# Kernel optimization log

Measured on AMD Instinct MI355X. Metric: run time of the kernel, lower is better.

The kernel has to match this reference:

```python
import jax, jax.numpy as jnp
import numpy as np

D_CONV = 4
DT_RANK = 64
D_STATE = 16

def silu(v):
    return v * jax.nn.sigmoid(v)

def setup_inputs() -> dict:
    key = jax.random.key(0)
    ks = jax.random.split(key, 10)
    B, L, d_model, d_inner = 2, 2048, 1024, 2048
    def nrm(k, shape, scale):
        return jax.random.normal(k, shape, dtype=jnp.float32) * scale
    A = jnp.tile(jnp.arange(1, D_STATE + 1, dtype=jnp.float32), (d_inner, 1))
    return {
        'x': nrm(ks[0], (B, L, d_model), 1.0),
        'W_in': nrm(ks[1], (d_model, 2 * d_inner), d_model ** -0.5),
        'conv_w': nrm(ks[2], (d_inner, D_CONV), D_CONV ** -0.5),
        'conv_b': nrm(ks[3], (d_inner,), 0.02),
        'W_x': nrm(ks[4], (d_inner, DT_RANK + 2 * D_STATE), d_inner ** -0.5),
        'W_dt': nrm(ks[5], (DT_RANK, d_inner), DT_RANK ** -0.5),
        'b_dt': nrm(ks[6], (d_inner,), 0.02),
        'A_log': jnp.log(A),
        'D': jnp.ones((d_inner,), dtype=jnp.float32),
        'W_out': nrm(ks[7], (d_inner, d_model), d_inner ** -0.5),
    }

def reference(x, W_in, conv_w, conv_b, W_x, W_dt, b_dt, A_log, D, W_out):
    B, L, _ = x.shape
    d_inner = W_dt.shape[1]
    # input projection and gate split
    xz = x @ W_in                                   # [B, L, 2*d_inner]
    xb, z = jnp.split(xz, 2, axis=-1)
    # causal depthwise conv1d (pad left d_conv-1, then first L outputs)
    xp = jnp.pad(xb, ((0, 0), (D_CONV - 1, 0), (0, 0)))
    xc = sum(xp[:, k:k + L, :] * conv_w[:, k] for k in range(D_CONV)) + conv_b
    xb = silu(xc)                                   # [B, L, d_inner]
    # data-dependent SSM parameters
    x_dbl = xb @ W_x                                # [B, L, dt_rank + 2*d_state]
    dt_low, Bm, Cm = jnp.split(x_dbl, [DT_RANK, DT_RANK + D_STATE], axis=-1)
    dt = jax.nn.softplus(dt_low @ W_dt + b_dt)      # [B, L, d_inner]
    A = -jnp.exp(A_log)                             # [d_inner, d_state]

    def step(h, inp):
        dt_t, B_t, C_t, x_t = inp                   # [B,d_inner],[B,n],[B,n],[B,d_inner]
        dA = jnp.exp(A * dt_t[..., None])           # [B, d_inner, d_state]
        h = h * dA + (x_t * dt_t)[..., None] * B_t[:, None, :]
        y = jnp.einsum('bdn,bn->bd', h, C_t)
        return h, y

    xs = (dt.swapaxes(0, 1), Bm.swapaxes(0, 1), Cm.swapaxes(0, 1), xb.swapaxes(0, 1))
    h0 = jnp.zeros((B, d_inner, D_STATE), dtype=x.dtype)
    _, ys = jax.lax.scan(step, h0, xs)              # ys: [L, B, d_inner]
    y = ys.swapaxes(0, 1) + xb * D
    out = y * silu(z)
    return out @ W_out
```

## Files before the change

kernel.cpp:

```cpp
#include <hip/hip_runtime.h>
#include <hip/hip_bf16.h>


#define BATCH   2
#define SEQLEN  2048
#define DMODEL  1024
#define DINNER  2048
#define DCONV   4
#define DTRANK  64
#define DSTATE  16
#define BL      (BATCH * SEQLEN)
#define NXZ     (2 * DINNER)
#define XDBL_N  (DTRANK + 2 * DSTATE)
#define LCH     32
#define NCHUNK  (SEQLEN / LCH)
#define KSPLIT  8
#define KC      (DINNER / KSPLIT)
#define KS_OUT  4
#define KCO     (DINNER / KS_OUT)
#define KS_XD   8
#define KCX     (DINNER / KS_XD)
#define XDP     128

typedef __bf16 bf16x8 __attribute__((ext_vector_type(8)));
typedef __bf16 bf16x4 __attribute__((ext_vector_type(4)));
typedef float  floatx4 __attribute__((ext_vector_type(4)));

__device__ __forceinline__ float silu_f(float v) {
    return v / (1.f + __expf(-v));
}

__device__ __forceinline__ float softplus_f(float v) {
    return (v > 20.f) ? v : __logf(1.f + __expf(v));
}

__device__ __forceinline__ float fast_exp2(float v) {
    return __builtin_amdgcn_exp2f(v);
}

__device__ __forceinline__ void gload_lds16(const __bf16* g, __bf16* l) {
    __builtin_amdgcn_global_load_lds(
        (const __attribute__((address_space(1))) void*)g,
        (__attribute__((address_space(3))) void*)l, 16, 0, 0);
}

#define VMW(n) asm volatile("s_waitcnt vmcnt(" #n ")" ::: "memory")
#define BARX() __builtin_amdgcn_s_barrier()

template <int BUF, int QA>
__device__ __forceinline__ void rdA(const char* rA, bf16x8 (&aF)[4][2]) {
#pragma unroll
    for (int j = 0; j < 4; ++j) {
        aF[j][0] = *(const bf16x8*)(rA + BUF * 65536 + ((QA * 4 + j) * 2 + 0) * 1024);
        aF[j][1] = *(const bf16x8*)(rA + BUF * 65536 + ((QA * 4 + j) * 2 + 1) * 1024);
    }
}

template <int BUF, int QB>
__device__ __forceinline__ void rdB(const char* rB, bf16x8 (&bF)[2][2]) {
#pragma unroll
    for (int f = 0; f < 2; ++f) {
        bF[f][0] = *(const bf16x8*)(rB + BUF * 65536 + QB * 8192 + f * 2048 + 0);
        bF[f][1] = *(const bf16x8*)(rB + BUF * 65536 + QB * 8192 + f * 2048 + 1024);
    }
}

template <int QA, int QB>
__device__ __forceinline__ void mf16(const bf16x8 (&aF)[4][2], const bf16x8 (&bF)[2][2],
                                     floatx4 (&acc)[8][4]) {
    __builtin_amdgcn_s_setprio(1);
#pragma unroll
    for (int ks = 0; ks < 2; ++ks)
#pragma unroll
        for (int j = 0; j < 4; ++j)
#pragma unroll
            for (int f = 0; f < 2; ++f)
                acc[QA * 4 + j][QB * 2 + f] = __builtin_amdgcn_mfma_f32_16x16x32_bf16(
                    aF[j][ks], bF[f][ks], acc[QA * 4 + j][QB * 2 + f], 0, 0, 0);
    __builtin_amdgcn_s_setprio(0);
}

template <int BUF, int QA>
__device__ __forceinline__ void stA2(const __bf16* gAs, char* sm, int lda, int w, int t) {
    gload_lds16(gAs + (size_t)(QA * 64) * lda + t * 64,
                (__bf16*)(sm + BUF * 65536 + QA * 8192 + w * 1024));
    gload_lds16(gAs + (size_t)(128 + QA * 64) * lda + t * 64,
                (__bf16*)(sm + BUF * 65536 + 16384 + QA * 8192 + w * 1024));
}

template <int BUF, int QB>
__device__ __forceinline__ void stB2(const __bf16* gBs, char* sm, int lda, int w, int t) {
    gload_lds16(gBs + (size_t)(QB * 32) * lda + t * 64,
                (__bf16*)(sm + BUF * 65536 + 32768 + QB * 8192 + w * 1024));
    gload_lds16(gBs + (size_t)(128 + QB * 32) * lda + t * 64,
                (__bf16*)(sm + BUF * 65536 + 32768 + 16384 + QB * 8192 + w * 1024));
}

template <int EPI>
__global__ __launch_bounds__(512, 2) void gemm_bt_256(
    const __bf16* __restrict__ A,
    const __bf16* __restrict__ BT,
    void* __restrict__ Cv,
    int M, int N, int K, int lda,
    const float* __restrict__ bias)
{
    __shared__ __align__(16) char smem[131072];

    const int tid  = threadIdx.x;
    const int w    = tid >> 6;
    const int lane = tid & 63;

    const int cpx = gridDim.x >> 3;
    const int swz = (blockIdx.x & 7) * cpx + (blockIdx.x >> 3);
    const int ntn = N >> 8;
    const int row0 = (swz / ntn) << 8;
    const int col0 = (swz % ntn) << 8;
    const int kbase = blockIdx.y * K;

    const int P     = tid;
    const int rr    = (P >> 2) & 15;
    const int qq    = (P & 3) ^ (2 * ((P >> 5) & 1));
    const int colE  = (((P >> 6) & 1) * 4 + qq) * 8;
    const int rgP   = P >> 7;
    const int rowAu = rgP * 16 + rr;
    const int rowBu = (rgP >> 1) * 64 + (rgP & 1) * 16 + rr;

    const __bf16* gAs = A  + (size_t)(row0 + rowAu) * lda + kbase + colE;
    const __bf16* gBs = BT + (size_t)(col0 + rowBu) * lda + kbase + colE;
    char* sm = smem;

    const int lsw = ((lane & 15) * 4 + ((lane >> 4) ^ (2 * ((lane >> 3) & 1)))) * 16;
    const char* rA = smem + (w >> 2) * 16384 + lsw;
    const char* rB = smem + 32768 + ((w & 3) >> 1) * 16384 + ((w & 3) & 1) * 4096 + lsw;

    floatx4 acc[8][4];
#pragma unroll
    for (int i = 0; i < 8; ++i)
#pragma unroll
        for (int j = 0; j < 4; ++j)
            acc[i][j] = (floatx4){0.f, 0.f, 0.f, 0.f};
    bf16x8 aF[4][2], bF[2][2];

    const int NT = K >> 6;
    const int NI = NT >> 1;

    stA2<0, 0>(gAs, sm, lda, w, 0);
    stB2<0, 0>(gBs, sm, lda, w, 0);
    stB2<0, 1>(gBs, sm, lda, w, 0);
    stA2<0, 1>(gAs, sm, lda, w, 0);
    stA2<1, 0>(gAs, sm, lda, w, 1);
    stB2<1, 1>(gBs, sm, lda, w, 1);
    VMW(6);
    BARX();

    for (int i = 0; i < NI - 1; ++i) {
        const int t1 = 2 * i + 1, t2 = 2 * i + 2, t3 = 2 * i + 3;
        rdA<0, 0>(rA, aF); rdB<0, 0>(rB, bF);
        stB2<1, 0>(gBs, sm, lda, w, t1);
        BARX(); mf16<0, 0>(aF, bF, acc); BARX();
        rdB<0, 1>(rB, bF);
        stA2<1, 1>(gAs, sm, lda, w, t1);
        BARX(); mf16<0, 1>(aF, bF, acc); VMW(8); BARX();
        rdA<0, 1>(rA, aF);
        stA2<0, 0>(gAs, sm, lda, w, t2);
        BARX(); mf16<1, 1>(aF, bF, acc); BARX();
        rdB<0, 0>(rB, bF);
        stB2<0, 1>(gBs, sm, lda, w, t2);
        BARX(); mf16<1, 0>(aF, bF, acc); VMW(6); BARX();
        rdA<1, 0>(rA, aF); rdB<1, 0>(rB, bF);
        stB2<0, 0>(gBs, sm, lda, w, t2);
        BARX(); mf16<0, 0>(aF, bF, acc); BARX();
        rdB<1, 1>(rB, bF);
        stA2<0, 1>(gAs, sm, lda, w, t2);
        BARX(); mf16<0, 1>(aF, bF, acc); VMW(8); BARX();
        rdA<1, 1>(rA, aF);
        stA2<1, 0>(gAs, sm, lda, w, t3);
        BARX(); mf16<1, 1>(aF, bF, acc); BARX();
        rdB<1, 0>(rB, bF);
        stB2<1, 1>(gBs, sm, lda, w, t3);
        BARX(); mf16<1, 0>(aF, bF, acc); VMW(6); BARX();
    }
    {
        const int t1 = NT - 1;
        rdA<0, 0>(rA, aF); rdB<0, 0>(rB, bF);
        stB2<1, 0>(gBs, sm, lda, w, t1);
        BARX(); mf16<0, 0>(aF, bF, acc); BARX();
        rdB<0, 1>(rB, bF);
        stA2<1, 1>(gAs, sm, lda, w, t1);
        BARX(); mf16<0, 1>(aF, bF, acc); VMW(8); BARX();
        rdA<0, 1>(rA, aF);
        BARX(); mf16<1, 1>(aF, bF, acc); BARX();
        rdB<0, 0>(rB, bF);
        BARX(); mf16<1, 0>(aF, bF, acc); VMW(2); BARX();
        rdA<1, 0>(rA, aF); rdB<1, 0>(rB, bF);
        BARX(); mf16<0, 0>(aF, bF, acc); BARX();
        rdB<1, 1>(rB, bF);
        BARX(); mf16<0, 1>(aF, bF, acc); VMW(0); BARX();
        rdA<1, 1>(rA, aF);
        BARX(); mf16<1, 1>(aF, bF, acc); BARX();
        rdB<1, 0>(rB, bF);
        BARX(); mf16<1, 0>(aF, bF, acc);
    }

    const int lrow = lane & 15, quad = lane >> 4;
    const int rbase = row0 + (w >> 2) * 128;
    const int cbase = col0 + (w & 3) * 64;
    const size_t cofs = (size_t)blockIdx.y * (size_t)M * (size_t)N;
#pragma unroll
    for (int fi = 0; fi < 8; ++fi) {
#pragma unroll
        for (int cf = 0; cf < 4; ++cf) {
            const int col = cbase + cf * 16 + lrow;
            const float bv = (EPI == 1 || EPI == 3) ? bias[col] : 0.f;
#pragma unroll
            for (int r = 0; r < 4; ++r) {
                const int row = rbase + fi * 16 + quad * 4 + r;
                float v = acc[fi][cf][r];
                if (EPI == 1 || EPI == 3) v = softplus_f(v + bv);
                if (EPI == 2 || EPI == 3)
                    ((__bf16*)Cv)[(size_t)row * N + col] = (__bf16)v;
                else
                    ((float*)Cv)[cofs + (size_t)row * N + col] = v;
            }
        }
    }
    (void)M;
}

__global__ __launch_bounds__(256) void out_reduce(
    const float* __restrict__ parts, float* __restrict__ out)
{
    const size_t i = ((size_t)blockIdx.x * 256 + threadIdx.x) * 4;
    floatx4 s = *(const floatx4*)(parts + i);
#pragma unroll
    for (int kz = 1; kz < KS_OUT; ++kz)
        s += *(const floatx4*)(parts + (size_t)kz * BL * DMODEL + i);
    *(floatx4*)(out + i) = s;
}

template <int EPI>
__global__ __launch_bounds__(256) void gemm_r64(
    const __bf16* __restrict__ A,
    const __bf16* __restrict__ BT,
    void* __restrict__ Cv,
    int M, int N, int K,
    const float* __restrict__ bias)
{
    __shared__ __bf16 Asm[64 * 32];
    __shared__ __bf16 Bsm[128 * 32];

    const int tid  = threadIdx.x;
    const int w    = tid >> 6;
    const int lane = tid & 63;
    const int lrow = lane & 15;
    const int quad = lane >> 4;
    const int row0 = blockIdx.y * 64;
    const int col0 = blockIdx.x * 128;
    const int wc   = w * 32;

    const int ldr = tid >> 2;
    const int ldk = (tid & 3) * 8;
    const __bf16* gA = A  + (size_t)(row0 + ldr) * K + ldk;
    const __bf16* gB = BT + (size_t)(col0 + ldr) * K + ldk;
    const size_t half = (size_t)64 * K;
    __bf16* lA0 = Asm + w * 512;
    __bf16* lB0 = Bsm + w * 512;
    __bf16* lB1 = Bsm + 2048 + w * 512;

    floatx4 acc[4][2];
#pragma unroll
    for (int i = 0; i < 4; ++i)
#pragma unroll
        for (int j = 0; j < 2; ++j)
            acc[i][j] = (floatx4){0.f, 0.f, 0.f, 0.f};

    for (int k0 = 0; k0 < K; k0 += 32) {
        gload_lds16(gA, lA0);
        gload_lds16(gB, lB0);
        gload_lds16(gB + half, lB1);
        gA += 32; gB += 32;
        __syncthreads();

        bf16x8 af[4], bf[2];
#pragma unroll
        for (int t = 0; t < 4; ++t)
            af[t] = *(const bf16x8*)(Asm + (t * 16 + lrow) * 32 + quad * 8);
#pragma unroll
        for (int u = 0; u < 2; ++u)
            bf[u] = *(const bf16x8*)(Bsm + (wc + u * 16 + lrow) * 32 + quad * 8);

#pragma unroll
        for (int ti = 0; ti < 4; ++ti)
#pragma unroll
            for (int tj = 0; tj < 2; ++tj)
                acc[ti][tj] = __builtin_amdgcn_mfma_f32_16x16x32_bf16(
                    af[ti], bf[tj], acc[ti][tj], 0, 0, 0);
        __syncthreads();
    }

#pragma unroll
    for (int ti = 0; ti < 4; ++ti) {
#pragma unroll
        for (int tj = 0; tj < 2; ++tj) {
            int col = col0 + wc + tj * 16 + lrow;
            float bv = (EPI == 1 || EPI == 3 || EPI == 4) ? bias[col] : 0.f;
            if (EPI == 4) {
                bf16x4 ov;
#pragma unroll
                for (int r = 0; r < 4; ++r)
                    ov[r] = (__bf16)softplus_f(acc[ti][tj][r] + bv);
                int rowb = row0 + ti * 16 + quad * 4;
                *(bf16x4*)((__bf16*)Cv + (size_t)col * M + rowb) = ov;
            } else {
#pragma unroll
                for (int r = 0; r < 4; ++r) {
                    int row = row0 + ti * 16 + quad * 4 + r;
                    float v = acc[ti][tj][r];
                    if (EPI == 1 || EPI == 3) v = softplus_f(v + bv);
                    if (EPI == 2 || EPI == 3)
                        ((__bf16*)Cv)[(size_t)row * N + col] = (__bf16)v;
                    else
                        ((float*)Cv)[(size_t)row * N + col] = v;
                }
            }
        }
    }
}

__global__ __launch_bounds__(256) void xdbl_gemm(
    const __bf16* __restrict__ A,
    const __bf16* __restrict__ BT,
    float* __restrict__ parts)
{
    __shared__ __bf16 Asm[64 * 32];
    __shared__ __bf16 Bsm[128 * 32];

    const int tid  = threadIdx.x;
    const int w    = tid >> 6;
    const int lane = tid & 63;
    const int lrow = lane & 15;
    const int quad = lane >> 4;
    const int row0 = blockIdx.x * 64;
    const int kbeg = blockIdx.y * KCX;
    const int wc   = w * 32;

    const int ldr = tid >> 2;
    const int ldk = (tid & 3) * 8;
    const __bf16* gA = A  + (size_t)(row0 + ldr) * DINNER + kbeg + ldk;
    const __bf16* gB = BT + (size_t)ldr * DINNER + kbeg + ldk;
    const size_t half = (size_t)64 * DINNER;
    __bf16* lA0 = Asm + w * 512;
    __bf16* lB0 = Bsm + w * 512;
    __bf16* lB1 = Bsm + 2048 + w * 512;

    floatx4 acc[4][2];
#pragma unroll
    for (int i = 0; i < 4; ++i)
#pragma unroll
        for (int j = 0; j < 2; ++j)
            acc[i][j] = (floatx4){0.f, 0.f, 0.f, 0.f};

    for (int k0 = 0; k0 < KCX; k0 += 32) {
        gload_lds16(gA, lA0);
        gload_lds16(gB, lB0);
        gload_lds16(gB + half, lB1);
        gA += 32; gB += 32;
        __syncthreads();

        bf16x8 af[4], bf[2];
#pragma unroll
        for (int t = 0; t < 4; ++t)
            af[t] = *(const bf16x8*)(Asm + (t * 16 + lrow) * 32 + quad * 8);
#pragma unroll
        for (int u = 0; u < 2; ++u)
            bf[u] = *(const bf16x8*)(Bsm + (wc + u * 16 + lrow) * 32 + quad * 8);

#pragma unroll
        for (int ti = 0; ti < 4; ++ti)
#pragma unroll
            for (int tj = 0; tj < 2; ++tj)
                acc[ti][tj] = __builtin_amdgcn_mfma_f32_16x16x32_bf16(
                    af[ti], bf[tj], acc[ti][tj], 0, 0, 0);
        __syncthreads();
    }

    const size_t base = (size_t)blockIdx.y * BL * XDP;
#pragma unroll
    for (int ti = 0; ti < 4; ++ti) {
#pragma unroll
        for (int tj = 0; tj < 2; ++tj) {
            int col = wc + tj * 16 + lrow;
#pragma unroll
            for (int r = 0; r < 4; ++r) {
                int row = row0 + ti * 16 + quad * 4 + r;
                parts[base + (size_t)row * XDP + col] = acc[ti][tj][r];
            }
        }
    }
}

__global__ __launch_bounds__(256) void xdbl_reduce2(
    const float* __restrict__ parts, float* __restrict__ xdbl,
    __bf16* __restrict__ dtlow16)
{
    const int i4  = blockIdx.x * 256 + threadIdx.x;
    const int row = i4 / 24;
    const int c4  = i4 - row * 24;
    const float* p = parts + (size_t)row * XDP + c4 * 4;
    floatx4 s = *(const floatx4*)p;
#pragma unroll
    for (int kz = 1; kz < KS_XD; ++kz)
        s += *(const floatx4*)(p + (size_t)kz * BL * XDP);
    *(floatx4*)(xdbl + (size_t)row * XDBL_N + c4 * 4) = s;
    if (c4 < 16) {
        bf16x4 o = {(__bf16)s.x, (__bf16)s.y, (__bf16)s.z, (__bf16)s.w};
        *(bf16x4*)(dtlow16 + (size_t)row * DTRANK + c4 * 4) = o;
    }
}

#define NB_CAST  ((BL * DMODEL / 4) / 256)
#define NB_WIN   ((NXZ / 32) * (DMODEL / 32))
#define NB_WOUT  ((DMODEL / 32) * (DINNER / 32))
#define NB_WDT   ((DINNER / 32) * (DTRANK / 32))
#define NB_CW    ((DCONV * DINNER) / 256)

__device__ __forceinline__ void transpose_tile(
    const float* __restrict__ src, __bf16* __restrict__ dst, int R, int Cc,
    int bx, int by, int tid, float* tile)
{
    int tx = tid & 31, ty = tid >> 5;
    int c0 = bx * 32, r0 = by * 32;
#pragma unroll
    for (int i = 0; i < 32; i += 8)
        tile[(ty + i) * 33 + tx] = src[(size_t)(r0 + ty + i) * Cc + c0 + tx];
    __syncthreads();
#pragma unroll
    for (int i = 0; i < 32; i += 8)
        dst[(size_t)(c0 + ty + i) * R + r0 + tx] = (__bf16)tile[tx * 33 + ty + i];
}

__global__ __launch_bounds__(256) void prep_kernel(
    const float* __restrict__ x,
    const float* __restrict__ W_in,
    const float* __restrict__ W_out,
    const float* __restrict__ W_dt,
    const float* __restrict__ conv_w,
    __bf16* __restrict__ xb16,
    __bf16* __restrict__ WiT16,
    __bf16* __restrict__ WoT16,
    __bf16* __restrict__ WdtT16,
    float* __restrict__ cwT)
{
    __shared__ float tile[32 * 33];
    const int tid = threadIdx.x;
    int bid = blockIdx.x;

    if (bid < NB_CAST) {
        long i = ((long)bid * 256 + tid) * 4;
        float4 v = *(const float4*)(x + i);
        bf16x4 o = {(__bf16)v.x, (__bf16)v.y, (__bf16)v.z, (__bf16)v.w};
        *(bf16x4*)(xb16 + i) = o;
        return;
    }
    bid -= NB_CAST;
    if (bid < NB_WIN) {
        transpose_tile(W_in, WiT16, DMODEL, NXZ,
                       bid % (NXZ / 32), bid / (NXZ / 32), tid, tile);
        return;
    }
    bid -= NB_WIN;
    if (bid < NB_WOUT) {
        transpose_tile(W_out, WoT16, DINNER, DMODEL,
                       bid % (DMODEL / 32), bid / (DMODEL / 32), tid, tile);
        return;
    }
    bid -= NB_WOUT;
    if (bid < NB_WDT) {
        transpose_tile(W_dt, WdtT16, DTRANK, DINNER,
                       bid % (DINNER / 32), bid / (DINNER / 32), tid, tile);
        return;
    }
    bid -= NB_WDT;
    {
        int i = bid * 256 + tid;
        int k = i / DINNER, d = i % DINNER;
        cwT[i] = conv_w[d * DCONV + k];
    }
}

#define NB_CONV  ((BL / 64) * KSPLIT)
#define NB_WXT   ((DINNER / 32) * (XDBL_N / 32))

__global__ __launch_bounds__(256) void conv_prep(
    const __bf16* __restrict__ xz16,
    const float* __restrict__ cwT,
    const float* __restrict__ cb,
    const float* __restrict__ W_x,
    __bf16* __restrict__ xc16,
    __bf16* __restrict__ xcT16,
    __bf16* __restrict__ WxT16)
{
    __shared__ float tile[32 * 33];
    const int tid = threadIdx.x;
    const int bid = blockIdx.x;

    if (bid >= NB_CONV) {
        const int b2 = bid - NB_CONV;
        transpose_tile(W_x, WxT16, DINNER, XDBL_N,
                       b2 % (XDBL_N / 32), b2 / (XDBL_N / 32), tid, tile);
        return;
    }

    const int row0 = (bid >> 3) * 64;
    const int kbeg = (bid & 7) * KC;
    const int ct = (tid & 31) * 8;
    const int rt = (tid >> 5) * 8;
    const int d  = kbeg + ct;

    float wreg[DCONV][8];
#pragma unroll
    for (int k = 0; k < DCONV; ++k) {
        float4 a = *(const float4*)(cwT + k * DINNER + d);
        float4 b = *(const float4*)(cwT + k * DINNER + d + 4);
        wreg[k][0]=a.x; wreg[k][1]=a.y; wreg[k][2]=a.z; wreg[k][3]=a.w;
        wreg[k][4]=b.x; wreg[k][5]=b.y; wreg[k][6]=b.z; wreg[k][7]=b.w;
    }
    float bias8[8];
    {
        float4 a = *(const float4*)(cb + d);
        float4 b = *(const float4*)(cb + d + 4);
        bias8[0]=a.x; bias8[1]=a.y; bias8[2]=a.z; bias8[3]=a.w;
        bias8[4]=b.x; bias8[5]=b.y; bias8[6]=b.z; bias8[7]=b.w;
    }

    const bf16x8 zero = {};
    bf16x8 win[DCONV];
    bf16x8 oT[8];
    const int tloc0 = (int)((row0 + rt) & (SEQLEN - 1));
#pragma unroll
    for (int j = 0; j < DCONV - 1; ++j)
        win[j] = (tloc0 - 3 + j >= 0)
            ? *(const bf16x8*)(xz16 + (size_t)(row0 + rt - 3 + j) * NXZ + d)
            : zero;

    for (int i = 0; i < 8; ++i) {
        size_t r = (size_t)row0 + rt + i;
        win[DCONV - 1] = *(const bf16x8*)(xz16 + r * NXZ + d);
        bf16x8 o;
#pragma unroll
        for (int j = 0; j < 8; ++j) {
            float acc = bias8[j];
#pragma unroll
            for (int k = 0; k < DCONV; ++k)
                acc += (float)win[k][j] * wreg[k][j];
            o[j] = (__bf16)silu_f(acc);
        }
        *(bf16x8*)(xc16 + r * DINNER + d) = o;
#pragma unroll
        for (int j = 0; j < 8; ++j) oT[j][i] = o[j];
#pragma unroll
        for (int k = 0; k < DCONV - 1; ++k)
            win[k] = win[k + 1];
    }
#pragma unroll
    for (int j = 0; j < 8; ++j)
        *(bf16x8*)(xcT16 + (size_t)(d + j) * BL + row0 + rt) = oT[j];
}

__global__ __launch_bounds__(256) void scan_pass1(
    const __bf16* __restrict__ dtT,
    const __bf16* __restrict__ xcT,
    const float* __restrict__ xdbl,
    const float* __restrict__ A_log,
    float* __restrict__ sums_h,
    float* __restrict__ sums_p)
{
    const int d  = blockIdx.x * 256 + threadIdx.x;
    const int bc = blockIdx.y;
    const int b  = bc / NCHUNK, c = bc % NCHUNK;
    const long r0 = (long)b * SEQLEN + (long)c * LCH;

    float Ad[DSTATE];
    {
        const float4* al = (const float4*)(A_log + d * DSTATE);
#pragma unroll
        for (int q = 0; q < 4; ++q) {
            float4 v = al[q];
            Ad[q * 4 + 0] = -__expf(v.x) * 1.44269504f;
            Ad[q * 4 + 1] = -__expf(v.y) * 1.44269504f;
            Ad[q * 4 + 2] = -__expf(v.z) * 1.44269504f;
            Ad[q * 4 + 3] = -__expf(v.w) * 1.44269504f;
        }
    }

    float h[DSTATE] = {};
    float Sdt = 0.f;
    const __bf16* pdt = dtT + (size_t)d * BL + r0;
    const __bf16* pxc = xcT + (size_t)d * BL + r0;
    const float*  pB  = xdbl + (size_t)r0 * XDBL_N + DTRANK;

    for (int g = 0; g < LCH / 8; ++g) {
        bf16x8 dt8 = *(const bf16x8*)(pdt + g * 8);
        bf16x8 xv8 = *(const bf16x8*)(pxc + g * 8);
#pragma unroll
        for (int u = 0; u < 8; ++u) {
            float dtv = (float)dt8[u];
            float xdt = (float)xv8[u] * dtv;
            Sdt += dtv;
            const float4* bv = (const float4*)(pB + (g * 8 + u) * XDBL_N);
            float4 B0 = bv[0], B1 = bv[1], B2 = bv[2], B3 = bv[3];
            const float Bn[DSTATE] = {B0.x,B0.y,B0.z,B0.w, B1.x,B1.y,B1.z,B1.w,
                                      B2.x,B2.y,B2.z,B2.w, B3.x,B3.y,B3.z,B3.w};
#pragma unroll
            for (int n = 0; n < DSTATE; ++n) {
                float dA = fast_exp2(Ad[n] * dtv);
                h[n] = h[n] * dA + xdt * Bn[n];
            }
        }
    }

    const long rowbase = (long)bc * DSTATE;
#pragma unroll
    for (int n = 0; n < DSTATE; ++n) {
        sums_h[(rowbase + n) * DINNER + d] = h[n];
        sums_p[(rowbase + n) * DINNER + d] = fast_exp2(Ad[n] * Sdt);
    }
}

__global__ __launch_bounds__(256) void scan_combine(
    float* __restrict__ sums_h, float* __restrict__ sums_p)
{
    int u = blockIdx.x * 256 + threadIdx.x;
    int d = u & (DINNER - 1);
    int n = (u >> 11) & (DSTATE - 1);
    int b = u >> 15;
    float hg = 0.f;
    for (int c = 0; c < NCHUNK; ++c) {
        long row = (long)(b * NCHUNK + c) * DSTATE + n;
        float p  = sums_p[row * DINNER + d];
        float hl = sums_h[row * DINNER + d];
        sums_p[row * DINNER + d] = hg;
        hg = p * hg + hl;
    }
}

__global__ __launch_bounds__(256) void scan_pass3(
    const __bf16* __restrict__ dtT,
    const __bf16* __restrict__ xcT,
    const float* __restrict__ xdbl,
    const float* __restrict__ A_log,
    const __bf16* __restrict__ xz16,
    const float* __restrict__ sums_p,
    const float* __restrict__ Dp,
    __bf16* __restrict__ gated)
{
    const int d  = blockIdx.x * 256 + threadIdx.x;
    const int bc = blockIdx.y;
    const int b  = bc / NCHUNK, c = bc % NCHUNK;
    const long r0 = (long)b * SEQLEN + (long)c * LCH;

    float Ad[DSTATE];
    {
        const float4* al = (const float4*)(A_log + d * DSTATE);
#pragma unroll
        for (int q = 0; q < 4; ++q) {
            float4 v = al[q];
            Ad[q * 4 + 0] = -__expf(v.x) * 1.44269504f;
            Ad[q * 4 + 1] = -__expf(v.y) * 1.44269504f;
            Ad[q * 4 + 2] = -__expf(v.z) * 1.44269504f;
            Ad[q * 4 + 3] = -__expf(v.w) * 1.44269504f;
        }
    }

    float h[DSTATE];
    const long rowbase = (long)bc * DSTATE;
#pragma unroll
    for (int n = 0; n < DSTATE; ++n)
        h[n] = sums_p[(rowbase + n) * DINNER + d];

    const float Dv = Dp[d];
    const __bf16* pdt = dtT + (size_t)d * BL + r0;
    const __bf16* pxc = xcT + (size_t)d * BL + r0;
    const float*  pBC = xdbl + (size_t)r0 * XDBL_N + DTRANK;
    const __bf16* pz  = xz16 + (size_t)r0 * NXZ + DINNER + d;
    __bf16*       pg  = gated + (size_t)r0 * DINNER + d;

    for (int g = 0; g < LCH / 8; ++g) {
        bf16x8 dt8 = *(const bf16x8*)(pdt + g * 8);
        bf16x8 xv8 = *(const bf16x8*)(pxc + g * 8);
#pragma unroll
        for (int u = 0; u < 8; ++u) {
            float dtv = (float)dt8[u];
            float xv  = (float)xv8[u];
            float xdt = xv * dtv;
            const float4* bv = (const float4*)(pBC + (g * 8 + u) * XDBL_N);
            float4 B0 = bv[0], B1 = bv[1], B2 = bv[2], B3 = bv[3];
            float4 C0 = bv[4], C1 = bv[5], C2 = bv[6], C3 = bv[7];
            const float Bn[DSTATE] = {B0.x,B0.y,B0.z,B0.w, B1.x,B1.y,B1.z,B1.w,
                                      B2.x,B2.y,B2.z,B2.w, B3.x,B3.y,B3.z,B3.w};
            const float Cn[DSTATE] = {C0.x,C0.y,C0.z,C0.w, C1.x,C1.y,C1.z,C1.w,
                                      C2.x,C2.y,C2.z,C2.w, C3.x,C3.y,C3.z,C3.w};
            float y = 0.f;
#pragma unroll
            for (int n = 0; n < DSTATE; ++n) {
                float dA = fast_exp2(Ad[n] * dtv);
                h[n] = h[n] * dA + xdt * Bn[n];
                y += h[n] * Cn[n];
            }
            float z = (float)pz[(size_t)(g * 8 + u) * NXZ];
            float yy = y + xv * Dv;
            pg[(size_t)(g * 8 + u) * DINNER] = (__bf16)(yy * silu_f(z));
        }
    }
}

extern "C" void kernel_launch(void* const* d_in, const int* in_sizes, int n_in,
                              void* d_out, int out_size, void* d_ws, size_t ws_size,
                              hipStream_t stream) {
    const float* x      = (const float*)d_in[0];
    const float* W_in   = (const float*)d_in[1];
    const float* conv_w = (const float*)d_in[2];
    const float* conv_b = (const float*)d_in[3];
    const float* W_x    = (const float*)d_in[4];
    const float* W_dt   = (const float*)d_in[5];
    const float* b_dt   = (const float*)d_in[6];
    const float* A_log  = (const float*)d_in[7];
    const float* Dp     = (const float*)d_in[8];
    const float* W_out  = (const float*)d_in[9];
    float* out = (float*)d_out;

    __bf16* xz16    = (__bf16*)d_ws;
    __bf16* xc16    = xz16 + (long)BL * NXZ;
    __bf16* dtT16   = xc16 + (long)BL * DINNER;
    __bf16* gated16 = dtT16 + (long)BL * DINNER;
    __bf16* WoT16   = gated16 + (long)BL * DINNER;
    __bf16* WdtT16  = WoT16 + (long)DINNER * DMODEL;
    __bf16* dtlow16 = WdtT16 + (long)DINNER * DTRANK;
    __bf16* xb16    = dtlow16 + (long)BL * DTRANK;
    __bf16* WiT16   = xb16 + (long)BL * DMODEL;
    float*  xdbl    = (float*)(WiT16 + (long)NXZ * DMODEL);
    float*  cwT     = xdbl + (long)BL * XDBL_N;
    float*  scratch = cwT + (long)DCONV * DINNER;
    float*  sums_h  = scratch;
    float*  sums_p  = scratch + (long)BATCH * NCHUNK * DSTATE * DINNER;
    __bf16* xcT16 = xb16;
    __bf16* WxT16 = (__bf16*)sums_p;
    float* outparts = (float*)d_ws;

    dim3 blk(256);

    prep_kernel<<<dim3(NB_CAST + NB_WIN + NB_WOUT + NB_WDT + NB_CW), blk, 0, stream>>>(
        x, W_in, W_out, W_dt, conv_w, xb16, WiT16, WoT16, WdtT16, cwT);

    gemm_bt_256<2><<<dim3((BL / 256) * (NXZ / 256)), dim3(512), 0, stream>>>(
        xb16, WiT16, xz16, BL, NXZ, DMODEL, DMODEL, nullptr);

    conv_prep<<<dim3(NB_CONV + NB_WXT), blk, 0, stream>>>(
        xz16, cwT, conv_b, W_x, xc16, xcT16, WxT16);

    xdbl_gemm<<<dim3(BL / 64, KS_XD), blk, 0, stream>>>(xc16, WxT16, scratch);
    xdbl_reduce2<<<dim3((BL * 24) / 256), blk, 0, stream>>>(scratch, xdbl, dtlow16);

    gemm_r64<4><<<dim3(DINNER / 128, BL / 64), blk, 0, stream>>>(
        dtlow16, WdtT16, dtT16, BL, DINNER, DTRANK, b_dt);

    {
        dim3 grid1(DINNER / 256, BATCH * NCHUNK);
        scan_pass1<<<grid1, blk, 0, stream>>>(dtT16, xcT16, xdbl, A_log,
                                              sums_h, sums_p);
        scan_combine<<<dim3((BATCH * DSTATE * DINNER) / 256), blk, 0, stream>>>(
            sums_h, sums_p);
        scan_pass3<<<grid1, blk, 0, stream>>>(dtT16, xcT16, xdbl, A_log, xz16,
                                              sums_p, Dp, gated16);
    }
    gemm_bt_256<0><<<dim3((BL / 256) * (DMODEL / 256), KS_OUT), dim3(512), 0, stream>>>(
        gated16, WoT16, outparts, BL, DMODEL, KCO, DINNER, nullptr);
    out_reduce<<<dim3((BL * DMODEL) / 1024), blk, 0, stream>>>(outparts, out);

    (void)in_sizes; (void)n_in; (void)out_size; (void)ws_size;
}
```

Baseline: 286.1 us.

## Stage GEMM epilogues through swizzled LDS and transpose dt GEMM operands

The 256-tile GEMM epilogue now writes accumulators into XOR-swizzled shared memory and then emits coalesced 16-byte row stores, for both the bf16 and the fp32 split-K outputs. The fp32 path runs in two halves to fit in LDS. The dt projection GEMM swaps its operands so it computes the transposed output directly, with a per-row bias softplus epilogue (EPI 5). This replaces the strided bf16x4 column-major stores. The cost is extra LDS traffic and barriers in exchange for better global write coalescing.

```diff
diff --git a/kernel.cpp b/kernel.cpp
--- a/kernel.cpp
+++ b/kernel.cpp
@@ -203,25 +203,67 @@
     }
 
     const int lrow = lane & 15, quad = lane >> 4;
-    const int rbase = row0 + (w >> 2) * 128;
-    const int cbase = col0 + (w & 3) * 64;
-    const size_t cofs = (size_t)blockIdx.y * (size_t)M * (size_t)N;
-#pragma unroll
-    for (int fi = 0; fi < 8; ++fi) {
-#pragma unroll
-        for (int cf = 0; cf < 4; ++cf) {
-            const int col = cbase + cf * 16 + lrow;
-            const float bv = (EPI == 1 || EPI == 3) ? bias[col] : 0.f;
-#pragma unroll
-            for (int r = 0; r < 4; ++r) {
-                const int row = rbase + fi * 16 + quad * 4 + r;
-                float v = acc[fi][cf][r];
-                if (EPI == 1 || EPI == 3) v = softplus_f(v + bv);
-                if (EPI == 2 || EPI == 3)
-                    ((__bf16*)Cv)[(size_t)row * N + col] = (__bf16)v;
-                else
-                    ((float*)Cv)[cofs + (size_t)row * N + col] = v;
+
+    if (EPI == 2 || EPI == 3) {
+        __syncthreads();
+#pragma unroll
+        for (int fi = 0; fi < 8; ++fi) {
+#pragma unroll
+            for (int cf = 0; cf < 4; ++cf) {
+                const int lc = (w & 3) * 64 + cf * 16 + lrow;
+                const float bv = (EPI == 3) ? bias[col0 + lc] : 0.f;
+#pragma unroll
+                for (int r = 0; r < 4; ++r) {
+                    const int lr = (w >> 2) * 128 + fi * 16 + quad * 4 + r;
+                    float v = acc[fi][cf][r];
+                    if (EPI == 3) v = softplus_f(v + bv);
+                    const int ck = (lc >> 3) ^ ((lr >> 2) & 7);
+                    *(__bf16*)(smem + lr * 512 + ck * 16 + (lc & 7) * 2) = (__bf16)v;
+                }
             }
+        }
+        __syncthreads();
+#pragma unroll
+        for (int it = 0; it < 16; ++it) {
+            const int row = it * 16 + w * 2 + (lane >> 5);
+            const int cr  = lane & 31;
+            const int ck  = cr ^ ((row >> 2) & 7);
+            bf16x8 v = *(const bf16x8*)(smem + row * 512 + ck * 16);
+            *(bf16x8*)((__bf16*)Cv + (size_t)(row0 + row) * N + col0 + cr * 8) = v;
+        }
+    } else {
+        const size_t cofs = (size_t)blockIdx.y * (size_t)M * (size_t)N;
+        __syncthreads();
+#pragma unroll
+        for (int half = 0; half < 2; ++half) {
+            if ((w >> 2) == half) {
+#pragma unroll
+                for (int fi = 0; fi < 8; ++fi) {
+#pragma unroll
+                    for (int cf = 0; cf < 4; ++cf) {
+                        const int lc = (w & 3) * 64 + cf * 16 + lrow;
+                        const float bv = (EPI == 1) ? bias[col0 + lc] : 0.f;
+#pragma unroll
+                        for (int r = 0; r < 4; ++r) {
+                            const int lr2 = fi * 16 + quad * 4 + r;
+                            float v = acc[fi][cf][r];
+                            if (EPI == 1) v = softplus_f(v + bv);
+                            const int ck = (lc >> 2) ^ (lr2 & 63);
+                            *(float*)(smem + lr2 * 1024 + ck * 16 + (lc & 3) * 4) = v;
+                        }
+                    }
+                }
+            }
+            __syncthreads();
+#pragma unroll
+            for (int it = 0; it < 16; ++it) {
+                const int row = it * 8 + w;
+                const int ck  = lane ^ (row & 63);
+                floatx4 v = *(const floatx4*)(smem + row * 1024 + ck * 16);
+                *(floatx4*)((float*)Cv + cofs +
+                            (size_t)(row0 + half * 128 + row) * N + col0 + lane * 4) = v;
+            }
+            __syncthreads();
         }
     }
     (void)M;
@@ -303,25 +345,17 @@
 #pragma unroll
         for (int tj = 0; tj < 2; ++tj) {
             int col = col0 + wc + tj * 16 + lrow;
-            float bv = (EPI == 1 || EPI == 3 || EPI == 4) ? bias[col] : 0.f;
-            if (EPI == 4) {
-                bf16x4 ov;
-#pragma unroll
-                for (int r = 0; r < 4; ++r)
-                    ov[r] = (__bf16)softplus_f(acc[ti][tj][r] + bv);
-                int rowb = row0 + ti * 16 + quad * 4;
-                *(bf16x4*)((__bf16*)Cv + (size_t)col * M + rowb) = ov;
-            } else {
-#pragma unroll
-                for (int r = 0; r < 4; ++r) {
-                    int row = row0 + ti * 16 + quad * 4 + r;
-                    float v = acc[ti][tj][r];
-                    if (EPI == 1 || EPI == 3) v = softplus_f(v + bv);
-                    if (EPI == 2 || EPI == 3)
-                        ((__bf16*)Cv)[(size_t)row * N + col] = (__bf16)v;
-                    else
-                        ((float*)Cv)[(size_t)row * N + col] = v;
-                }
+            float bv = (EPI == 1 || EPI == 3) ? bias[col] : 0.f;
+#pragma unroll
+            for (int r = 0; r < 4; ++r) {
+                int row = row0 + ti * 16 + quad * 4 + r;
+                float v = acc[ti][tj][r];
+                if (EPI == 1 || EPI == 3) v = softplus_f(v + bv);
+                if (EPI == 5)            v = softplus_f(v + bias[row]);
+                if (EPI == 2 || EPI == 3 || EPI == 5)
+                    ((__bf16*)Cv)[(size_t)row * N + col] = (__bf16)v;
+                else
+                    ((float*)Cv)[(size_t)row * N + col] = v;
             }
         }
     }
@@ -761,8 +795,8 @@
     xdbl_gemm<<<dim3(BL / 64, KS_XD), blk, 0, stream>>>(xc16, WxT16, scratch);
     xdbl_reduce2<<<dim3((BL * 24) / 256), blk, 0, stream>>>(scratch, xdbl, dtlow16);
 
-    gemm_r64<4><<<dim3(DINNER / 128, BL / 64), blk, 0, stream>>>(
-        dtlow16, WdtT16, dtT16, BL, DINNER, DTRANK, b_dt);
+    gemm_r64<5><<<dim3(BL / 128, DINNER / 64), blk, 0, stream>>>(
+        WdtT16, dtlow16, dtT16, DINNER, BL, DTRANK, b_dt);
 
     {
         dim3 grid1(DINNER / 256, BATCH * NCHUNK);
```

Result: slower. 293.2 us (+2.5%).
